# Performance work log

Hardware: AMD Instinct MI355X
Metric: run time of the kernel (lower is better)

The kernel has to match this reference:

```python
import jax, jax.numpy as jnp
import numpy as np


def _skew(w):
    # w: (..., 3) -> (..., 3, 3)
    wx, wy, wz = w[..., 0], w[..., 1], w[..., 2]
    z = jnp.zeros_like(wx)
    return jnp.stack([
        jnp.stack([z, -wz, wy], axis=-1),
        jnp.stack([wz, z, -wx], axis=-1),
        jnp.stack([-wy, wx, z], axis=-1),
    ], axis=-2)


def exp_se3(xi):
    # xi: (..., 6) se(3) coordinates [w, v] -> (..., 4, 4) SE(3) matrix exponential
    w = xi[..., :3]
    v = xi[..., 3:]
    th2 = jnp.sum(w * w, axis=-1)
    small = th2 < 1e-12
    th2_safe = jnp.where(small, 1.0, th2)
    th = jnp.sqrt(th2_safe)
    # Rodrigues coefficients with small-angle Taylor fallbacks
    A = jnp.where(small, 1.0 - th2 / 6.0, jnp.sin(th) / th)
    B = jnp.where(small, 0.5 - th2 / 24.0, (1.0 - jnp.cos(th)) / th2_safe)
    C = jnp.where(small, 1.0 / 6.0 - th2 / 120.0, (th - jnp.sin(th)) / (th2_safe * th))
    W = _skew(w)
    W2 = W @ W
    I3 = jnp.eye(3, dtype=xi.dtype)
    R = I3 + A[..., None, None] * W + B[..., None, None] * W2
    V = I3 + B[..., None, None] * W + C[..., None, None] * W2
    p = jnp.einsum('...ij,...j->...i', V, v)
    top = jnp.concatenate([R, p[..., None]], axis=-1)            # (..., 3, 4)
    bottom_row = jnp.array([0.0, 0.0, 0.0, 1.0], dtype=xi.dtype)
    bot = jnp.broadcast_to(bottom_row, top.shape[:-2] + (1, 4))  # (..., 1, 4)
    return jnp.concatenate([top, bot], axis=-2)


def setup_inputs() -> dict:
    key = jax.random.key(0)
    k1, k2, k3 = jax.random.split(key, 3)
    nBatch, nJoint = 262144, 24
    x = jax.random.normal(k1, (nBatch, nJoint), dtype=jnp.float32)
    # eta ~ U(-1, 1) per torch init (stdv = 1)
    eta = jax.random.uniform(k2, (nJoint, 6), dtype=jnp.float32, minval=-1.0, maxval=1.0)
    # M_se3 ~ U(-2, 2)
    M_se3 = jax.random.uniform(k3, (1, 6), dtype=jnp.float32, minval=-2.0, maxval=2.0)
    return {"x": x, "eta": eta, "M_se3": M_se3}


def reference(x, eta, M_se3):
    # x: (B, nJoint) joint angles; eta: (nJoint, 6) joint twists (useAdjoint=False);
    # M_se3: (1, 6) home pose in se(3).
    nBatch = x.shape[0]
    joint_twist = eta  # getJointTwist() with useAdjoint=False

    def step(T, inp):
        twist, ang = inp                                  # (6,), (B,)
        E = exp_se3(ang[:, None] * twist[None, :])        # (B, 4, 4)
        return T @ E, None

    T0 = jnp.broadcast_to(jnp.eye(4, dtype=x.dtype), (nBatch, 4, 4))
    T, _ = jax.lax.scan(step, T0, (joint_twist, x.T))
    return T @ exp_se3(M_se3)  # (B,4,4) @ (1,4,4) broadcasts over batch
```

## Files before the change

### kernel.cpp

```cpp
#include <hip/hip_runtime.h>

#define NJ   24
#define BLK  256
#define JREC 5
#define QMF4 (NJ * JREC)
#define NCPY (NJ * JREC + 2)
#define INV4PI 0.07957747154594767f

struct DQ { float w, x, y, z, t0, t1, t2; };

__device__ __forceinline__ DQ dq_comp(const DQ A, const DQ B) {
    const float u10 = A.y*B.t2 - A.z*B.t1;
    const float u11 = A.z*B.t0 - A.x*B.t2;
    const float u12 = A.x*B.t1 - A.y*B.t0;
    const float u20 = A.y*u12 - A.z*u11;
    const float u21 = A.z*u10 - A.x*u12;
    const float u22 = A.x*u11 - A.y*u10;
    const float tw  = 2.0f * A.w;
    DQ C;
    C.t0 = fmaf(tw, u10, fmaf(2.0f, u20, A.t0 + B.t0));
    C.t1 = fmaf(tw, u11, fmaf(2.0f, u21, A.t1 + B.t1));
    C.t2 = fmaf(tw, u12, fmaf(2.0f, u22, A.t2 + B.t2));
    C.w = A.w*B.w - A.x*B.x - A.y*B.y - A.z*B.z;
    C.x = A.w*B.x + A.x*B.w + A.y*B.z - A.z*B.y;
    C.y = A.w*B.y - A.x*B.z + A.y*B.w + A.z*B.x;
    C.z = A.w*B.z + A.x*B.y - A.y*B.x + A.z*B.w;
    return C;
}

__device__ __forceinline__ DQ dq_exp(const float4 A4, const float4 B4,
                                     const float4 C4, const float4 D4,
                                     const float a) {
    const float hrev = a * B4.w;
    const float sh   = __builtin_amdgcn_sinf(hrev);
    const float ch   = __builtin_amdgcn_cosf(hrev);
    const float s    = 2.0f * sh * ch;
    const float cB   = 2.0f * sh * sh;
    const float phi  = a * A4.w;
    const float g    = phi - s;
    DQ e;
    e.w  = ch;
    e.x  = sh * A4.x;
    e.y  = sh * A4.y;
    e.z  = sh * A4.z;
    e.t0 = fmaf(a, B4.x, fmaf(cB, C4.x, g * D4.x));
    e.t1 = fmaf(a, B4.y, fmaf(cB, C4.y, g * D4.y));
    e.t2 = fmaf(a, B4.z, fmaf(cB, C4.z, g * D4.z));
    return e;
}

__global__ __launch_bounds__(BLK, 4)
void poe_main(const float* __restrict__ x,
              const float* __restrict__ eta,
              const float* __restrict__ M,
              float* __restrict__ out,
              int nBatch)
{
    __shared__ float4 sC[NCPY];
    float* sF = (float*)sC;

    const int t = threadIdx.x;
    if (t < NJ) {
        const float w0 = eta[t*6+0], w1 = eta[t*6+1], w2 = eta[t*6+2];
        const float v0 = eta[t*6+3], v1 = eta[t*6+4], v2 = eta[t*6+5];
        const float k  = w0*w0 + w1*w1 + w2*w2;
        const bool  sm = (k < 1e-12f);
        const float invsqk = sm ? 0.0f : rsqrtf(k);
        const float sqk    = k * invsqk;
        const float invk   = invsqk * invsqk;
        const float invk15 = invk * invsqk;
        const float c10 = w1*v2 - w2*v1;
        const float c11 = w2*v0 - w0*v2;
        const float c12 = w0*v1 - w1*v0;
        const float c20 = w1*c12 - w2*c11;
        const float c21 = w2*c10 - w0*c12;
        const float c22 = w0*c11 - w1*c10;
        float* r = sF + t * JREC * 4;
        r[0]  = w0*invsqk;  r[1]  = w1*invsqk;  r[2]  = w2*invsqk;  r[3]  = sqk;
        r[4]  = v0;         r[5]  = v1;         r[6]  = v2;         r[7]  = sqk * INV4PI;
        r[8]  = c10*invk;   r[9]  = c11*invk;   r[10] = c12*invk;   r[11] = 0.0f;
        r[12] = c20*invk15; r[13] = c21*invk15; r[14] = c22*invk15; r[15] = 0.0f;
    } else if (t == NJ) {
        const float w0 = M[0], w1 = M[1], w2 = M[2];
        const float v0 = M[3], v1 = M[4], v2 = M[5];
        const float t2 = w0*w0 + w1*w1 + w2*w2;
        const bool  sm = (t2 < 1e-12f);
        const float t2s  = sm ? 1.0f : t2;
        const float invt = rsqrtf(t2s);
        const float th   = t2s * invt;
        float s, c;
        __sincosf(th, &s, &c);
        const float invt2 = invt * invt;
        const float B = sm ? 0.5f        : (1.0f - c) * invt2;
        const float C = sm ? (1.0f/6.0f) : (th - s) * invt2 * invt;
        float sh, chh;
        __sincosf(0.5f * th, &sh, &chh);
        const float axs = sm ? 0.5f : sh * invt;
        float* r = sF + QMF4 * 4;
        r[0] = sm ? 1.0f : chh;
        r[1] = axs * w0;
        r[2] = axs * w1;
        r[3] = axs * w2;
        const float c10 = w1*v2 - w2*v1, c11 = w2*v0 - w0*v2, c12 = w0*v1 - w1*v0;
        const float c20 = w1*c12 - w2*c11, c21 = w2*c10 - w0*c12, c22 = w0*c11 - w1*c10;
        r[4] = v0 + B*c10 + C*c20;
        r[5] = v1 + B*c11 + C*c21;
        r[6] = v2 + B*c12 + C*c22;
        r[7] = 0.0f;
    }

    const int gid = blockIdx.x * BLK + t;
    const int row = gid >> 2;
    const int q   = gid & 3;
    const bool active = row < nBatch;

    float2 xa = make_float2(0.f,0.f), xb = xa, xc = xa;
    if (active) {
        const float2* xp = (const float2*)(x + (size_t)row * NJ + q * 6);
        xa = xp[0]; xb = xp[1]; xc = xp[2];
    }

    __syncthreads();

    const int cbase = q * 6 * JREC;

#define REC(JJ, S) sC[cbase + (JJ)*JREC + (S)]

    const DQ e0 = dq_exp(REC(0,0), REC(0,1), REC(0,2), REC(0,3), xa.x);
    const DQ e1 = dq_exp(REC(1,0), REC(1,1), REC(1,2), REC(1,3), xa.y);
    const DQ e2 = dq_exp(REC(2,0), REC(2,1), REC(2,2), REC(2,3), xb.x);
    const DQ e3 = dq_exp(REC(3,0), REC(3,1), REC(3,2), REC(3,3), xb.y);
    const DQ e4 = dq_exp(REC(4,0), REC(4,1), REC(4,2), REC(4,3), xc.x);
    const DQ e5 = dq_exp(REC(5,0), REC(5,1), REC(5,2), REC(5,3), xc.y);
#undef REC

    const DQ c01 = dq_comp(e0, e1);
    const DQ c23 = dq_comp(e2, e3);
    const DQ c45 = dq_comp(e4, e5);
    const DQ c03 = dq_comp(c01, c23);
    DQ T = dq_comp(c03, c45);

#define COMBINE(BIT) do {                                                     \
    DQ O;                                                                     \
    O.w  = __shfl_xor(T.w,  BIT);  O.x  = __shfl_xor(T.x,  BIT);              \
    O.y  = __shfl_xor(T.y,  BIT);  O.z  = __shfl_xor(T.z,  BIT);              \
    O.t0 = __shfl_xor(T.t0, BIT);  O.t1 = __shfl_xor(T.t1, BIT);              \
    O.t2 = __shfl_xor(T.t2, BIT);                                             \
    const bool up = (q & (BIT)) != 0;          \
    DQ A, B;                                                                  \
    A.w  = up ? O.w  : T.w;   B.w  = up ? T.w  : O.w;                         \
    A.x  = up ? O.x  : T.x;   B.x  = up ? T.x  : O.x;                         \
    A.y  = up ? O.y  : T.y;   B.y  = up ? T.y  : O.y;                         \
    A.z  = up ? O.z  : T.z;   B.z  = up ? T.z  : O.z;                         \
    A.t0 = up ? O.t0 : T.t0;  B.t0 = up ? T.t0 : O.t0;                        \
    A.t1 = up ? O.t1 : T.t1;  B.t1 = up ? T.t1 : O.t1;                        \
    A.t2 = up ? O.t2 : T.t2;  B.t2 = up ? T.t2 : O.t2;                        \
    T = dq_comp(A, B);                                                        \
} while (0)

    COMBINE(1);
    COMBINE(2);
#undef COMBINE

    {
        const float4 Qm = sC[QMF4];
        const float4 Pm = sC[QMF4 + 1];
        DQ Em;
        Em.w = Qm.x; Em.x = Qm.y; Em.y = Qm.z; Em.z = Qm.w;
        Em.t0 = Pm.x; Em.t1 = Pm.y; Em.t2 = Pm.z;
        T = dq_comp(T, Em);
    }

    if (active) {
        const float xx = T.x*T.x, yy = T.y*T.y, zz = T.z*T.z;
        const float xy = T.x*T.y, xz = T.x*T.z, yz = T.y*T.z;
        const float wx = T.w*T.x, wy = T.w*T.y, wz = T.w*T.z;
        const float R00 = 1.0f - 2.0f*(yy + zz);
        const float R01 = 2.0f*(xy - wz);
        const float R02 = 2.0f*(xz + wy);
        const float R10 = 2.0f*(xy + wz);
        const float R11 = 1.0f - 2.0f*(xx + zz);
        const float R12 = 2.0f*(yz - wx);
        const float R20 = 2.0f*(xz - wy);
        const float R21 = 2.0f*(yz + wx);
        const float R22 = 1.0f - 2.0f*(xx + yy);

        float4 mine;
        if      (q == 0) mine = make_float4(R00, R01, R02, T.t0);
        else if (q == 1) mine = make_float4(R10, R11, R12, T.t1);
        else if (q == 2) mine = make_float4(R20, R21, R22, T.t2);
        else             mine = make_float4(0.0f, 0.0f, 0.0f, 1.0f);

        ((float4*)out)[(size_t)row * 4 + q] = mine;
    }
}

extern "C" void kernel_launch(void* const* d_in, const int* in_sizes, int n_in,
                              void* d_out, int out_size, void* d_ws, size_t ws_size,
                              hipStream_t stream)
{
    const float* x   = (const float*)d_in[0];
    const float* eta = (const float*)d_in[1];
    const float* M   = (const float*)d_in[2];
    float* out = (float*)d_out;

    const int nBatch   = in_sizes[0] / NJ;
    const int nThreads = nBatch * 4;
    const int grid     = (nThreads + BLK - 1) / BLK;

    poe_main<<<grid, BLK, 0, stream>>>(x, eta, M, out, nBatch);
}
```

Baseline: 21.24 us.

## Split each batch row across two threads and combine halves with DPP moves

```diff
diff --git a/kernel.cpp b/kernel.cpp
--- a/kernel.cpp
+++ b/kernel.cpp
@@ -2,12 +2,19 @@
 
 #define NJ   24
 #define BLK  256
-#define JREC 5
-#define QMF4 (NJ * JREC)
-#define NCPY (NJ * JREC + 2)
+#define QMF4 (NJ * 4)
+#define NCPY (NJ * 4 + 2)
 #define INV4PI 0.07957747154594767f
+#define FOURPI 12.566370614359172f
 
 struct DQ { float w, x, y, z, t0, t1, t2; };
+
+template<int CTRL>
+__device__ __forceinline__ float dppmov(float v) {
+    return __int_as_float(__builtin_amdgcn_mov_dpp(__float_as_int(v), CTRL, 0xF, 0xF, true));
+}
+#define DPP_LO 0xA0
+#define DPP_HI 0xF5
 
 __device__ __forceinline__ DQ dq_comp(const DQ A, const DQ B) {
     const float u10 = A.y*B.t2 - A.z*B.t1;
@@ -28,27 +35,6 @@
     return C;
 }
 
-__device__ __forceinline__ DQ dq_exp(const float4 A4, const float4 B4,
-                                     const float4 C4, const float4 D4,
-                                     const float a) {
-    const float hrev = a * B4.w;
-    const float sh   = __builtin_amdgcn_sinf(hrev);
-    const float ch   = __builtin_amdgcn_cosf(hrev);
-    const float s    = 2.0f * sh * ch;
-    const float cB   = 2.0f * sh * sh;
-    const float phi  = a * A4.w;
-    const float g    = phi - s;
-    DQ e;
-    e.w  = ch;
-    e.x  = sh * A4.x;
-    e.y  = sh * A4.y;
-    e.z  = sh * A4.z;
-    e.t0 = fmaf(a, B4.x, fmaf(cB, C4.x, g * D4.x));
-    e.t1 = fmaf(a, B4.y, fmaf(cB, C4.y, g * D4.y));
-    e.t2 = fmaf(a, B4.z, fmaf(cB, C4.z, g * D4.z));
-    return e;
-}
-
 __global__ __launch_bounds__(BLK, 4)
 void poe_main(const float* __restrict__ x,
               const float* __restrict__ eta,
@@ -75,7 +61,7 @@
         const float c20 = w1*c12 - w2*c11;
         const float c21 = w2*c10 - w0*c12;
         const float c22 = w0*c11 - w1*c10;
-        float* r = sF + t * JREC * 4;
+        float* r = sF + t * 16;
         r[0]  = w0*invsqk;  r[1]  = w1*invsqk;  r[2]  = w2*invsqk;  r[3]  = sqk;
         r[4]  = v0;         r[5]  = v1;         r[6]  = v2;         r[7]  = sqk * INV4PI;
         r[8]  = c10*invk;   r[9]  = c11*invk;   r[10] = c12*invk;   r[11] = 0.0f;
@@ -98,69 +84,80 @@
         const float axs = sm ? 0.5f : sh * invt;
         float* r = sF + QMF4 * 4;
         r[0] = sm ? 1.0f : chh;
-        r[1] = axs * w0;
-        r[2] = axs * w1;
-        r[3] = axs * w2;
-        const float c10 = w1*v2 - w2*v1, c11 = w2*v0 - w0*v2, c12 = w0*v1 - w1*v0;
-        const float c20 = w1*c12 - w2*c11, c21 = w2*c10 - w0*c12, c22 = w0*c11 - w1*c10;
-        r[4] = v0 + B*c10 + C*c20;
-        r[5] = v1 + B*c11 + C*c21;
-        r[6] = v2 + B*c12 + C*c22;
+        r[1] = axs * w0;  r[2] = axs * w1;  r[3] = axs * w2;
+        const float a0 = w1*v2 - w2*v1, a1 = w2*v0 - w0*v2, a2 = w0*v1 - w1*v0;
+        const float b0 = w1*a2 - w2*a1, b1 = w2*a0 - w0*a2, b2 = w0*a1 - w1*a0;
+        r[4] = v0 + B*a0 + C*b0;
+        r[5] = v1 + B*a1 + C*b1;
+        r[6] = v2 + B*a2 + C*b2;
         r[7] = 0.0f;
     }
 
     const int gid = blockIdx.x * BLK + t;
-    const int row = gid >> 2;
-    const int q   = gid & 3;
+    const int row = gid >> 1;
+    const int h   = gid & 1;
     const bool active = row < nBatch;
 
-    float2 xa = make_float2(0.f,0.f), xb = xa, xc = xa;
+    float4 xz4 = make_float4(0.f,0.f,0.f,0.f);
+    float4 xa = xz4, xb = xz4, xc = xz4;
     if (active) {
-        const float2* xp = (const float2*)(x + (size_t)row * NJ + q * 6);
+        const float4* xp = (const float4*)(x + (size_t)row * NJ + h * 12);
         xa = xp[0]; xb = xp[1]; xc = xp[2];
     }
 
     __syncthreads();
 
-    const int cbase = q * 6 * JREC;
-
-#define REC(JJ, S) sC[cbase + (JJ)*JREC + (S)]
-
-    const DQ e0 = dq_exp(REC(0,0), REC(0,1), REC(0,2), REC(0,3), xa.x);
-    const DQ e1 = dq_exp(REC(1,0), REC(1,1), REC(1,2), REC(1,3), xa.y);
-    const DQ e2 = dq_exp(REC(2,0), REC(2,1), REC(2,2), REC(2,3), xb.x);
-    const DQ e3 = dq_exp(REC(3,0), REC(3,1), REC(3,2), REC(3,3), xb.y);
-    const DQ e4 = dq_exp(REC(4,0), REC(4,1), REC(4,2), REC(4,3), xc.x);
-    const DQ e5 = dq_exp(REC(5,0), REC(5,1), REC(5,2), REC(5,3), xc.y);
-#undef REC
-
-    const DQ c01 = dq_comp(e0, e1);
-    const DQ c23 = dq_comp(e2, e3);
-    const DQ c45 = dq_comp(e4, e5);
-    const DQ c03 = dq_comp(c01, c23);
-    DQ T = dq_comp(c03, c45);
-
-#define COMBINE(BIT) do {                                                     \
-    DQ O;                                                                     \
-    O.w  = __shfl_xor(T.w,  BIT);  O.x  = __shfl_xor(T.x,  BIT);              \
-    O.y  = __shfl_xor(T.y,  BIT);  O.z  = __shfl_xor(T.z,  BIT);              \
-    O.t0 = __shfl_xor(T.t0, BIT);  O.t1 = __shfl_xor(T.t1, BIT);              \
-    O.t2 = __shfl_xor(T.t2, BIT);                                             \
-    const bool up = (q & (BIT)) != 0;          \
-    DQ A, B;                                                                  \
-    A.w  = up ? O.w  : T.w;   B.w  = up ? T.w  : O.w;                         \
-    A.x  = up ? O.x  : T.x;   B.x  = up ? T.x  : O.x;                         \
-    A.y  = up ? O.y  : T.y;   B.y  = up ? T.y  : O.y;                         \
-    A.z  = up ? O.z  : T.z;   B.z  = up ? T.z  : O.z;                         \
-    A.t0 = up ? O.t0 : T.t0;  B.t0 = up ? T.t0 : O.t0;                        \
-    A.t1 = up ? O.t1 : T.t1;  B.t1 = up ? T.t1 : O.t1;                        \
-    A.t2 = up ? O.t2 : T.t2;  B.t2 = up ? T.t2 : O.t2;                        \
-    T = dq_comp(A, B);                                                        \
+    const int cbase = h * 48;
+    DQ T;
+
+#define JSTEP(JJ, A_, FIRST) do {                                             \
+    const float4 A4 = sC[cbase + (JJ)*4 + 0];                                 \
+    const float4 B4 = sC[cbase + (JJ)*4 + 1];                                 \
+    const float4 C4 = sC[cbase + (JJ)*4 + 2];                                 \
+    const float4 D4 = sC[cbase + (JJ)*4 + 3];                                 \
+    const float a    = (A_);                                                  \
+    const float hrev = a * B4.w;                                              \
+    const float sh   = __builtin_amdgcn_sinf(hrev);                           \
+    const float ch   = __builtin_amdgcn_cosf(hrev);                           \
+    const float s    = 2.0f * sh * ch;                        \
+    const float cB   = 2.0f * sh * sh;                        \
+    const float g    = fmaf(FOURPI, hrev, -s);              \
+    DQ e;                                                                     \
+    e.w  = ch;                                                                \
+    e.x  = sh * A4.x;                                                         \
+    e.y  = sh * A4.y;                                                         \
+    e.z  = sh * A4.z;                                                         \
+    e.t0 = fmaf(a, B4.x, fmaf(cB, C4.x, g * D4.x));                           \
+    e.t1 = fmaf(a, B4.y, fmaf(cB, C4.y, g * D4.y));                           \
+    e.t2 = fmaf(a, B4.z, fmaf(cB, C4.z, g * D4.z));                           \
+    if (FIRST) T = e; else T = dq_comp(T, e);                                 \
 } while (0)
 
-    COMBINE(1);
-    COMBINE(2);
-#undef COMBINE
+    JSTEP( 0, xa.x, true);
+    JSTEP( 1, xa.y, false);
+    JSTEP( 2, xa.z, false);
+    JSTEP( 3, xa.w, false);
+    JSTEP( 4, xb.x, false);
+    JSTEP( 5, xb.y, false);
+    JSTEP( 6, xb.z, false);
+    JSTEP( 7, xb.w, false);
+    JSTEP( 8, xc.x, false);
+    JSTEP( 9, xc.y, false);
+    JSTEP(10, xc.z, false);
+    JSTEP(11, xc.w, false);
+#undef JSTEP
+
+    {
+        DQ A, B;
+        A.w  = dppmov<DPP_LO>(T.w);   B.w  = dppmov<DPP_HI>(T.w);
+        A.x  = dppmov<DPP_LO>(T.x);   B.x  = dppmov<DPP_HI>(T.x);
+        A.y  = dppmov<DPP_LO>(T.y);   B.y  = dppmov<DPP_HI>(T.y);
+        A.z  = dppmov<DPP_LO>(T.z);   B.z  = dppmov<DPP_HI>(T.z);
+        A.t0 = dppmov<DPP_LO>(T.t0);  B.t0 = dppmov<DPP_HI>(T.t0);
+        A.t1 = dppmov<DPP_LO>(T.t1);  B.t1 = dppmov<DPP_HI>(T.t1);
+        A.t2 = dppmov<DPP_LO>(T.t2);  B.t2 = dppmov<DPP_HI>(T.t2);
+        T = dq_comp(A, B);
+    }
 
     {
         const float4 Qm = sC[QMF4];
@@ -173,25 +170,16 @@
 
     if (active) {
         const float xx = T.x*T.x, yy = T.y*T.y, zz = T.z*T.z;
-        const float xy = T.x*T.y, xz = T.x*T.z, yz = T.y*T.z;
+        const float xy = T.x*T.y, xzp = T.x*T.z, yz = T.y*T.z;
         const float wx = T.w*T.x, wy = T.w*T.y, wz = T.w*T.z;
-        const float R00 = 1.0f - 2.0f*(yy + zz);
-        const float R01 = 2.0f*(xy - wz);
-        const float R02 = 2.0f*(xz + wy);
-        const float R10 = 2.0f*(xy + wz);
-        const float R11 = 1.0f - 2.0f*(xx + zz);
-        const float R12 = 2.0f*(yz - wx);
-        const float R20 = 2.0f*(xz - wy);
-        const float R21 = 2.0f*(yz + wx);
-        const float R22 = 1.0f - 2.0f*(xx + yy);
-
-        float4 mine;
-        if      (q == 0) mine = make_float4(R00, R01, R02, T.t0);
-        else if (q == 1) mine = make_float4(R10, R11, R12, T.t1);
-        else if (q == 2) mine = make_float4(R20, R21, R22, T.t2);
-        else             mine = make_float4(0.0f, 0.0f, 0.0f, 1.0f);
-
-        ((float4*)out)[(size_t)row * 4 + q] = mine;
+        float4* o = (float4*)(out + (size_t)row * 16);
+        if (h == 0) {
+            o[0] = make_float4(1.0f-2.0f*(yy+zz), 2.0f*(xy-wz),      2.0f*(xzp+wy),     T.t0);
+            o[1] = make_float4(2.0f*(xy+wz),      1.0f-2.0f*(xx+zz), 2.0f*(yz-wx),      T.t1);
+        } else {
+            o[2] = make_float4(2.0f*(xzp-wy),     2.0f*(yz+wx),      1.0f-2.0f*(xx+yy), T.t2);
+            o[3] = make_float4(0.0f, 0.0f, 0.0f, 1.0f);
+        }
     }
 }
 
@@ -205,7 +193,7 @@
     float* out = (float*)d_out;
 
     const int nBatch   = in_sizes[0] / NJ;
-    const int nThreads = nBatch * 4;
+    const int nThreads = nBatch * 2;
     const int grid     = (nThreads + BLK - 1) / BLK;
 
     poe_main<<<grid, BLK, 0, stream>>>(x, eta, M, out, nBatch);
```

After: 24.28 us. 14.3% more time.
